# Performance work log

Measured on AMD Instinct MI355X. Metric: run time of the kernel, lower is better.

Reference implementation:

```python
import jax, jax.numpy as jnp
import numpy as np

N = 2048      # agent_num
H = 2048      # hid_size
OBS = 1024    # obs_size
A = 64        # action_dim
ITERS = 3     # comm_iters
B = 1         # batch (structurally 1: original does gate.view(1,n,n))
STD = 0.02


def setup_inputs() -> dict:
    key = jax.random.key(0)
    ks = jax.random.split(key, 10)
    f = lambda k, shp: (jax.random.normal(k, shp, jnp.float32) * STD)
    return {
        "obs": jax.random.normal(ks[0], (B, N, OBS), jnp.float32),
        "alive_mask": jnp.ones((N,), jnp.float32),
        "enc_w": f(ks[1], (H, OBS)),
        "enc_b": jnp.zeros((H,), jnp.float32),
        "g_w": f(ks[2], (N, H)),
        "g_b": jnp.zeros((N,), jnp.float32),
        "w_ih": f(ks[3], (4 * H, H)),
        "w_hh": f(ks[4], (4 * H, H)),
        "b_ih": f(ks[5], (4 * H,)),
        "b_hh": f(ks[6], (4 * H,)),
        "act_w": f(ks[7], (A, H)),
        "act_b": jnp.zeros((A,), jnp.float32),
        "val_w": f(ks[8], (1, H)),
        "val_b": jnp.zeros((1,), jnp.float32),
    }


def reference(obs, alive_mask, enc_w, enc_b, g_w, g_b, w_ih, w_hh,
              b_ih, b_hh, act_w, act_b, val_w, val_b):
    b, n, _ = obs.shape
    hid = enc_w.shape[0]
    # state encoder: tanh(Linear(obs))
    e = jnp.tanh(jnp.einsum('bno,ho->bnh', obs, enc_w) + enc_b)  # (B,n,H)
    h = jnp.zeros((b, n, hid), obs.dtype)
    cell = jnp.zeros((b, n, hid), obs.dtype)
    comm_mask = 1.0 - jnp.eye(n, dtype=obs.dtype)                # (n,n), no self-comm
    n_alive = jnp.sum(alive_mask)
    alive_pair = alive_mask[:, None] * alive_mask[None, :]       # alive[j]*alive[i]
    static_w = comm_mask * alive_pair / (n_alive - 1.0)          # (n,n)

    for it in range(ITERS):
        # hard gate: ceil(sigmoid(g(h)))  -> (B, n_sender, n_receiver)
        gate = jnp.ceil(jax.nn.sigmoid(jnp.einsum('bjh,kh->bjk', h, g_w) + g_b))
        G = gate * static_w                                      # (B,n,n)
        # masked gated broadcast-sum over sender agents j (fused, no (B,n,n,H))
        if it == 0:
            c = jnp.zeros_like(h)
        else:
            c = jnp.einsum('bji,bjh->bih', G, h)
        inp = e + c                                              # (B,n,H)
        # torch.nn.LSTMCell, gate order (i, f, g, o)
        z = (jnp.einsum('bnh,gh->bng', inp, w_ih)
             + jnp.einsum('bnh,gh->bng', h, w_hh) + b_ih + b_hh)
        zi, zf, zg, zo = jnp.split(z, 4, axis=-1)
        cell = jax.nn.sigmoid(zf) * cell + jax.nn.sigmoid(zi) * jnp.tanh(zg)
        h = jax.nn.sigmoid(zo) * jnp.tanh(cell)

    log_p = jax.nn.log_softmax(jnp.einsum('bnh,ah->bna', h, act_w) + act_b, axis=-1)
    value = jnp.einsum('bnh,vh->bnv', h, val_w) + val_b
    return log_p, value
```

## Files before the change

### kernel.cpp

```cpp
#include <hip/hip_runtime.h>
#include <cmath>

#define N_AG 2048
#define HID  2048
#define OBSD 1024
#define ACT  64
#define GATES (4*HID)

typedef short s16x8 __attribute__((ext_vector_type(8)));
typedef short s16x4 __attribute__((ext_vector_type(4)));
typedef float f32x4 __attribute__((ext_vector_type(4)));

__device__ __forceinline__ unsigned short f2bf(float f) {
  union { float f; unsigned u; } v; v.f = f;
  return (unsigned short)((v.u + 0x7FFFu + ((v.u >> 16) & 1u)) >> 16);
}
__device__ __forceinline__ float bf2f(unsigned short u) {
  union { float f; unsigned u; } v; v.u = ((unsigned)u) << 16;
  return v.f;
}
__device__ __forceinline__ float sigm(float x) { return 1.0f / (1.0f + expf(-x)); }

__device__ __forceinline__ void gload16(const unsigned short* g, unsigned short* l) {
  __builtin_amdgcn_global_load_lds(
      (const __attribute__((address_space(1))) void*)g,
      (__attribute__((address_space(3))) void*)l, 16, 0, 0);
}

__global__ __launch_bounds__(512, 2) void gemm256(
    const unsigned short* __restrict__ A, const unsigned short* __restrict__ B,
    int K, int lda, int ldb, unsigned short* __restrict__ C, int ldc)
{
  __shared__ __align__(16) unsigned short As[32768];
  __shared__ __align__(16) unsigned short Bs[32768];

  const int tid  = threadIdx.x;
  const int lane = tid & 63;
  const int wave = tid >> 6;
  const int wm   = wave >> 2, wn = wave & 3;
  const int quad = lane >> 4, l16 = lane & 15, r7 = lane & 7;
  const long tileM = (long)blockIdx.y * 256;
  const long tileN = (long)blockIdx.x * 256;

  const unsigned scol = (((lane & 7) ^ (lane >> 3)) * 8u);
  unsigned aoff[2][2], boff[2][2];
#pragma unroll
  for (int c = 0; c < 2; ++c)
#pragma unroll
    for (int h = 0; h < 2; ++h) {
      unsigned ar = c * 128u + h * 64u + wave * 8u + (lane >> 3);
      unsigned br = c * 128u + (wave >> 2) * 64u + h * 32u + (wave & 3) * 8u + (lane >> 3);
      aoff[c][h] = (unsigned)(tileM + ar) * (unsigned)lda + scol;
      boff[c][h] = (unsigned)(tileN + br) * (unsigned)ldb + scol;
    }

#define ST_A(d, h, t) { \
    gload16(A + aoff[0][h] + (unsigned)(t) * 64u, &As[(d) * 16384 + (h) * 8192 + wave * 512]); \
    gload16(A + aoff[1][h] + (unsigned)(t) * 64u, &As[(d) * 16384 + (h) * 8192 + wave * 512 + 4096]); }
#define ST_B(d, h, t) { \
    gload16(B + boff[0][h] + (unsigned)(t) * 64u, &Bs[(d) * 16384 + (h) * 8192 + wave * 512]); \
    gload16(B + boff[1][h] + (unsigned)(t) * 64u, &Bs[(d) * 16384 + (h) * 8192 + wave * 512 + 4096]); }

  const int ax = wm * 4096 + l16 * 64;
  const int bx = wn * 2048 + l16 * 64;
  const int c0 = (quad ^ r7) * 8;
  const int c1 = ((4 + quad) ^ r7) * 8;

  s16x8 af[4][2], bA[2][2], bB[2][2];
  f32x4 acc[8][4] = {};

#define LD_A(d, Mh) { const unsigned short* p_ = &As[(d) * 16384 + (Mh) * 8192 + ax]; \
    _Pragma("unroll") for (int ml = 0; ml < 4; ++ml) { \
      af[ml][0] = *(const s16x8*)(p_ + ml * 1024 + c0); \
      af[ml][1] = *(const s16x8*)(p_ + ml * 1024 + c1); } }
#define LD_B(d, Nh, bb) { const unsigned short* p_ = &Bs[(d) * 16384 + (Nh) * 8192 + bx]; \
    _Pragma("unroll") for (int nl = 0; nl < 2; ++nl) { \
      bb[nl][0] = *(const s16x8*)(p_ + nl * 1024 + c0); \
      bb[nl][1] = *(const s16x8*)(p_ + nl * 1024 + c1); } }
#define QMM(Mh, Nh, bb) \
    _Pragma("unroll") for (int ml = 0; ml < 4; ++ml) \
    _Pragma("unroll") for (int nl = 0; nl < 2; ++nl) \
    _Pragma("unroll") for (int ks = 0; ks < 2; ++ks) \
      acc[(Mh) * 4 + ml][(Nh) * 2 + nl] = __builtin_amdgcn_mfma_f32_16x16x32_bf16( \
          af[ml][ks], bb[nl][ks], acc[(Mh) * 4 + ml][(Nh) * 2 + nl], 0, 0, 0);
#define LGKM0 asm volatile("s_waitcnt lgkmcnt(0)" ::: "memory")
#define BARRIER __builtin_amdgcn_s_barrier()

  const int NT = K >> 6;

  ST_B(0, 0, 0); ST_A(0, 0, 0); ST_B(0, 1, 0); ST_A(0, 1, 0);
  ST_B(1, 0, 1); ST_A(1, 0, 1); ST_B(1, 1, 1);
  asm volatile("s_waitcnt vmcnt(6)" ::: "memory");
  BARRIER;

  for (int t = 0; t < NT; ++t) {
    const int cur = t & 1, nxt = cur ^ 1;
    const bool s1 = (t + 1 < NT), s2 = (t + 2 < NT);
    LD_A(cur, 0); LD_B(cur, 0, bA);
    if (s1) ST_A(nxt, 1, t + 1);
    BARRIER; LGKM0;
    __builtin_amdgcn_s_setprio(1); QMM(0, 0, bA); __builtin_amdgcn_s_setprio(0);
    BARRIER;
    LD_B(cur, 1, bB);
    if (s2) ST_B(cur, 0, t + 2);
    BARRIER; LGKM0;
    __builtin_amdgcn_s_setprio(1); QMM(0, 1, bB); __builtin_amdgcn_s_setprio(0);
    BARRIER;
    LD_A(cur, 1);
    if (s2) ST_A(cur, 0, t + 2);
    BARRIER; LGKM0;
    __builtin_amdgcn_s_setprio(1); QMM(1, 0, bA); __builtin_amdgcn_s_setprio(0);
    BARRIER;
    if (s2) ST_B(cur, 1, t + 2);
    BARRIER; LGKM0;
    __builtin_amdgcn_s_setprio(1); QMM(1, 1, bB); __builtin_amdgcn_s_setprio(0);
    if (s2)      { asm volatile("s_waitcnt vmcnt(6)" ::: "memory"); }
    else if (s1) { asm volatile("s_waitcnt vmcnt(0)" ::: "memory"); }
    BARRIER;
  }

#pragma unroll
  for (int mf = 0; mf < 8; ++mf) {
    long r0 = tileM + wm * 128 + mf * 16 + quad * 4;
#pragma unroll
    for (int nf = 0; nf < 4; ++nf) {
      long col = tileN + wn * 64 + nf * 16 + l16;
#pragma unroll
      for (int r = 0; r < 4; ++r)
        C[(r0 + r) * ldc + col] = f2bf(acc[mf][nf][r]);
    }
  }
#undef ST_A
#undef ST_B
#undef LD_A
#undef LD_B
#undef QMM
#undef LGKM0
#undef BARRIER
}

template <int MODE>
__global__ __launch_bounds__(256, 4) void gemm_bt(
    const unsigned short* __restrict__ A, const unsigned short* __restrict__ B,
    int K, int lda, int ldb,
    unsigned short* __restrict__ Cb, float* __restrict__ Cf, int ldc,
    const float* __restrict__ bias)
{
  __shared__ __align__(16) unsigned short As0[2 * 128 * 32];
  __shared__ __align__(16) unsigned short Bs0[2 * 128 * 32];
  const int tid  = threadIdx.x;
  const int lane = tid & 63;
  const int wave = tid >> 6;
  const int wm = wave >> 1, wn = wave & 1;
  const int quad = lane >> 4, l16 = lane & 15;
  const long tileM = (long)blockIdx.y * 128;
  const long tileN = (long)blockIdx.x * 128;

  const int srow = lane >> 2;
  const int skc  = (lane & 3) * 8;
  const unsigned short* gA = &A[(tileM + wave * 32 + srow) * lda + skc];
  const unsigned short* gB = &B[(tileN + wave * 32 + srow) * ldb + skc];
  const int ldsOff = wave * 32 * 32;

  f32x4 acc[4][4] = {};
  const int nIt = K >> 5;

  gload16(gA, &As0[ldsOff]);
  gload16(gA + 16 * lda, &As0[ldsOff + 16 * 32]);
  gload16(gB, &Bs0[ldsOff]);
  gload16(gB + 16 * ldb, &Bs0[ldsOff + 16 * 32]);

  for (int i = 0; i < nIt; ++i) {
    __syncthreads();
    const int cb = (i & 1) * 4096;
    if (i + 1 < nIt) {
      const int nb = ((i + 1) & 1) * 4096;
      const long ko = (long)(i + 1) * 32;
      gload16(gA + ko, &As0[nb + ldsOff]);
      gload16(gA + ko + 16 * lda, &As0[nb + ldsOff + 16 * 32]);
      gload16(gB + ko, &Bs0[nb + ldsOff]);
      gload16(gB + ko + 16 * ldb, &Bs0[nb + ldsOff + 16 * 32]);
    }
    s16x8 af[4], bfr[4];
#pragma unroll
    for (int ii = 0; ii < 4; ++ii)
      af[ii] = *(const s16x8*)&As0[cb + (wm * 64 + ii * 16 + l16) * 32 + quad * 8];
#pragma unroll
    for (int j = 0; j < 4; ++j)
      bfr[j] = *(const s16x8*)&Bs0[cb + (wn * 64 + j * 16 + l16) * 32 + quad * 8];
#pragma unroll
    for (int ii = 0; ii < 4; ++ii)
#pragma unroll
      for (int j = 0; j < 4; ++j)
        acc[ii][j] = __builtin_amdgcn_mfma_f32_16x16x32_bf16(af[ii], bfr[j], acc[ii][j], 0, 0, 0);
  }

#pragma unroll
  for (int i = 0; i < 4; ++i) {
    long r0 = tileM + wm * 64 + i * 16 + quad * 4;
#pragma unroll
    for (int j = 0; j < 4; ++j) {
      long col = tileN + wn * 64 + j * 16 + l16;
      float bv = (MODE == 1) ? bias[col] : 0.f;
#pragma unroll
      for (int r = 0; r < 4; ++r) {
        float v = acc[i][j][r];
        if (MODE == 1) v = tanhf(v + bv);
        if (MODE == 2) Cf[(r0 + r) * ldc + col] = v;
        else           Cb[(r0 + r) * ldc + col] = f2bf(v);
      }
    }
  }
}

__global__ void cvt4_dual(const float* __restrict__ inA, unsigned short* __restrict__ outA,
                          const float* __restrict__ inB, unsigned short* __restrict__ outB) {
  int i = blockIdx.x * 256 + threadIdx.x;
  f32x4 a = ((const f32x4*)inA)[i];
  f32x4 b = ((const f32x4*)inB)[i];
  s16x4 oa, ob;
#pragma unroll
  for (int c = 0; c < 4; ++c) { oa[c] = (short)f2bf(a[c]); ob[c] = (short)f2bf(b[c]); }
  ((s16x4*)outA)[i] = oa;
  ((s16x4*)outB)[i] = ob;
}

__global__ void buildw(const float* __restrict__ w_ih, const float* __restrict__ w_hh,
                       const float* __restrict__ nA,
                       unsigned short* __restrict__ Wihb, unsigned short* __restrict__ W2b) {
  int i = blockIdx.x * 256 + threadIdx.x;
  float s = 1.0f / (nA[0] - 1.0f);
  size_t off = (size_t)i * 4;
  f32x4 a = *(const f32x4*)&w_ih[off];
  f32x4 b = *(const f32x4*)&w_hh[off];
  s16x4 oa, ob;
#pragma unroll
  for (int c = 0; c < 4; ++c) {
    oa[c] = (short)f2bf(a[c]);
    ob[c] = (short)f2bf(b[c] - s * a[c]);
  }
  *(s16x4*)&Wihb[off] = oa;
  *(s16x4*)&W2b[off] = ob;
}

__global__ void build_whd(const float* __restrict__ act_w, const float* __restrict__ val_w,
                          unsigned short* __restrict__ whd) {
  int i = blockIdx.x * 256 + threadIdx.x;
  int r = i >> 9;
  int k = (i & 511) * 4;
  f32x4 v = {0.f, 0.f, 0.f, 0.f};
  if (r < 64)       v = *(const f32x4*)&act_w[(size_t)r * HID + k];
  else if (r == 64) v = *(const f32x4*)&val_w[k];
  s16x4 o;
  o[0] = (short)f2bf(v[0]); o[1] = (short)f2bf(v[1]);
  o[2] = (short)f2bf(v[2]); o[3] = (short)f2bf(v[3]);
  *(s16x4*)&whd[(size_t)r * HID + k] = o;
}

__global__ void biasmix(const float* __restrict__ b_ih, const float* __restrict__ b_hh,
                        float* __restrict__ bc) {
  int i = blockIdx.x * 256 + threadIdx.x;
  if (i < GATES) bc[i] = b_ih[i] + b_hh[i];
}

__global__ void nalive_k(const float* __restrict__ alive, float* __restrict__ nA) {
  __shared__ float red[256];
  float s = 0.f;
  for (int i = threadIdx.x; i < N_AG; i += 256) s += alive[i];
  red[threadIdx.x] = s;
  __syncthreads();
  for (int st = 128; st > 0; st >>= 1) {
    if (threadIdx.x < st) red[threadIdx.x] += red[threadIdx.x + st];
    __syncthreads();
  }
  if (threadIdx.x == 0) nA[0] = red[0];
}

__global__ void colsum(const unsigned short* __restrict__ hb, const float* __restrict__ alive,
                       float* __restrict__ S) {
  int hid = blockIdx.x * 256 + threadIdx.x;
  int r0 = blockIdx.y * 128;
  float s = 0.f;
  for (int n = r0; n < r0 + 128; ++n) s += alive[n] * bf2f(hb[(size_t)n * HID + hid]);
  atomicAdd(&S[hid], s);
}

__global__ __launch_bounds__(256) void gemv_q(const unsigned short* __restrict__ Wihb,
                                              const float* __restrict__ S,
                                              const float* __restrict__ nA,
                                              float* __restrict__ q) {
  __shared__ float Sl[HID];
  int tid = threadIdx.x, lane = tid & 63, wave = tid >> 6;
  for (int k = tid; k < HID; k += 256) Sl[k] = S[k];
  __syncthreads();
  int g = blockIdx.x * 4 + wave;
  const unsigned short* wr = Wihb + (size_t)g * HID;
  float acc = 0.f;
#pragma unroll
  for (int c = 0; c < 4; ++c) {
    int k = c * 512 + lane * 8;
    s16x8 w = *(const s16x8*)&wr[k];
#pragma unroll
    for (int e = 0; e < 8; ++e) acc += bf2f((unsigned short)w[e]) * Sl[k + e];
  }
  for (int off = 32; off; off >>= 1) acc += __shfl_xor(acc, off);
  if (lane == 0) q[g] = acc / (nA[0] - 1.0f);
}

__global__ void lstm_k(const unsigned short* __restrict__ zb, const unsigned short* __restrict__ E1b,
                       const float* __restrict__ q, const float* __restrict__ bc,
                       float* __restrict__ cell, unsigned short* __restrict__ hb, int first) {
  int i = blockIdx.x * 256 + threadIdx.x;
  int n = i >> 9;
  int hid = (i & 511) * 4;
  size_t base = (size_t)n * GATES;
  float zt[4][4];
#pragma unroll
  for (int t = 0; t < 4; ++t) {
    int off = t * HID + hid;
    s16x4 e1 = *(const s16x4*)&E1b[base + off];
    f32x4 bcv = *(const f32x4*)&bc[off];
#pragma unroll
    for (int c = 0; c < 4; ++c) zt[t][c] = bf2f((unsigned short)e1[c]) + bcv[c];
    if (!first) {
      s16x4 z2 = *(const s16x4*)&zb[base + off];
      f32x4 qv = *(const f32x4*)&q[off];
#pragma unroll
      for (int c = 0; c < 4; ++c) zt[t][c] += bf2f((unsigned short)z2[c]) + qv[c];
    }
  }
  f32x4 cold = {0.f, 0.f, 0.f, 0.f};
  if (!first) cold = ((const f32x4*)cell)[i];
  f32x4 cnew; s16x4 xb;
#pragma unroll
  for (int c = 0; c < 4; ++c) {
    float ig = sigm(zt[0][c]);
    float fg = sigm(zt[1][c]);
    float gg = tanhf(zt[2][c]);
    float og = sigm(zt[3][c]);
    cnew[c] = fg * cold[c] + ig * gg;
    float hv = og * tanhf(cnew[c]);
    xb[c] = (short)f2bf(hv);
  }
  ((f32x4*)cell)[i] = cnew;
  *(s16x4*)&hb[(size_t)n * HID + hid] = xb;
}

__global__ __launch_bounds__(256) void head_ep(const float* __restrict__ zh,
                                               const float* __restrict__ act_b,
                                               const float* __restrict__ val_b,
                                               float* __restrict__ out) {
  int wave = threadIdx.x >> 6, lane = threadIdx.x & 63;
  int row = blockIdx.x * 4 + wave;
  const float* zr = zh + (size_t)row * 128;
  float a = zr[lane] + act_b[lane];
  float m = a;
  for (int off = 32; off; off >>= 1) m = fmaxf(m, __shfl_xor(m, off));
  float ex = expf(a - m), s = ex;
  for (int off = 32; off; off >>= 1) s += __shfl_xor(s, off);
  out[(size_t)row * ACT + lane] = a - m - logf(s);
  if (lane == 0) out[(size_t)N_AG * ACT + row] = zr[64] + val_b[0];
}

extern "C" void kernel_launch(void* const* d_in, const int* in_sizes, int n_in,
                              void* d_out, int out_size, void* d_ws, size_t ws_size,
                              hipStream_t stream) {
  const float* obs   = (const float*)d_in[0];
  const float* alive = (const float*)d_in[1];
  const float* enc_w = (const float*)d_in[2];
  const float* enc_b = (const float*)d_in[3];
  const float* w_ih  = (const float*)d_in[6];
  const float* w_hh  = (const float*)d_in[7];
  const float* b_ih  = (const float*)d_in[8];
  const float* b_hh  = (const float*)d_in[9];
  const float* act_w = (const float*)d_in[10];
  const float* act_b = (const float*)d_in[11];
  const float* val_w = (const float*)d_in[12];
  const float* val_b = (const float*)d_in[13];
  float* out = (float*)d_out;

  char* p = (char*)d_ws;
  unsigned short* Wihb = (unsigned short*)p; p += (size_t)GATES * HID * 2;
  unsigned short* W2b  = (unsigned short*)p; p += (size_t)GATES * HID * 2;
  unsigned short* E1b  = (unsigned short*)p; p += (size_t)N_AG * GATES * 2;
  unsigned short* zb   = (unsigned short*)p; p += (size_t)N_AG * GATES * 2;
  unsigned short* obsb = (unsigned short*)p; p += (size_t)N_AG * OBSD * 2;
  unsigned short* encb = (unsigned short*)p; p += (size_t)HID * OBSD * 2;
  unsigned short* eb   = (unsigned short*)p; p += (size_t)N_AG * HID * 2;
  unsigned short* hb   = (unsigned short*)p; p += (size_t)N_AG * HID * 2;
  unsigned short* Whd  = (unsigned short*)p; p += (size_t)128 * HID * 2;
  float* cell = (float*)p; p += (size_t)N_AG * HID * 4;
  float* zh   = (float*)p; p += (size_t)N_AG * 128 * 4;
  float* bc   = (float*)p; p += GATES * 4;
  float* q    = (float*)p; p += GATES * 4;
  float* S    = (float*)p; p += HID * 4;
  float* nA   = (float*)p; p += 256;

  cvt4_dual<<<(N_AG * OBSD / 4) / 256, 256, 0, stream>>>(obs, obsb, enc_w, encb);
  nalive_k<<<1, 256, 0, stream>>>(alive, nA);
  buildw<<<((size_t)GATES * HID / 4) / 256, 256, 0, stream>>>(w_ih, w_hh, nA, Wihb, W2b);
  build_whd<<<(128 * HID / 4) / 256, 256, 0, stream>>>(act_w, val_w, Whd);
  biasmix<<<GATES / 256, 256, 0, stream>>>(b_ih, b_hh, bc);

  gemm_bt<1><<<dim3(HID / 128, N_AG / 128), 256, 0, stream>>>(
      obsb, encb, OBSD, OBSD, OBSD, eb, nullptr, HID, enc_b);

  gemm256<<<dim3(GATES / 256, N_AG / 256), 512, 0, stream>>>(
      eb, Wihb, HID, HID, HID, E1b, GATES);
  lstm_k<<<(N_AG * HID / 4) / 256, 256, 0, stream>>>(nullptr, E1b, nullptr, bc, cell, hb, 1);

  for (int it = 1; it < 3; ++it) {
    hipMemsetAsync(S, 0, HID * 4, stream);
    colsum<<<dim3(HID / 256, 16), 256, 0, stream>>>(hb, alive, S);
    gemv_q<<<GATES / 4, 256, 0, stream>>>(Wihb, S, nA, q);
    gemm256<<<dim3(GATES / 256, N_AG / 256), 512, 0, stream>>>(
        hb, W2b, HID, HID, HID, zb, GATES);
    lstm_k<<<(N_AG * HID / 4) / 256, 256, 0, stream>>>(zb, E1b, q, bc, cell, hb, 0);
  }

  gemm_bt<2><<<dim3(1, N_AG / 128), 256, 0, stream>>>(
      hb, Whd, HID, HID, HID, nullptr, zh, 128, nullptr);
  head_ep<<<N_AG / 4, 256, 0, stream>>>(zh, act_b, val_b, out);
}
```

Baseline: 564.4 us.

## Double-buffer A fragments in registers and cut barriers in gemm256 loop

Rewrites the main loop of the 256x256 bf16 MFMA GEMM so that LDS fragment reads for the next quarter-tile, and for the next k-tile, are issued before the current MFMA block runs. A second A-fragment register set (af0/af1) makes this possible. The explicit lgkmcnt waits and roughly half of the workgroup barriers are removed, and the end-of-iteration global-load wait is loosened to vmcnt(2). Per-lane global offsets are now computed from one base address instead of held in eight precomputed registers. The goal is to hide LDS latency and cut synchronization stalls, at the cost of more live vector registers under a 512x2 launch bound and a greater risk of LDS races or spills.

```diff
diff --git a/kernel.cpp b/kernel.cpp
--- a/kernel.cpp
+++ b/kernel.cpp
@@ -42,81 +42,73 @@
   const long tileM = (long)blockIdx.y * 256;
   const long tileN = (long)blockIdx.x * 256;
 
-  const unsigned scol = (((lane & 7) ^ (lane >> 3)) * 8u);
-  unsigned aoff[2][2], boff[2][2];
-#pragma unroll
-  for (int c = 0; c < 2; ++c)
-#pragma unroll
-    for (int h = 0; h < 2; ++h) {
-      unsigned ar = c * 128u + h * 64u + wave * 8u + (lane >> 3);
-      unsigned br = c * 128u + (wave >> 2) * 64u + h * 32u + (wave & 3) * 8u + (lane >> 3);
-      aoff[c][h] = (unsigned)(tileM + ar) * (unsigned)lda + scol;
-      boff[c][h] = (unsigned)(tileN + br) * (unsigned)ldb + scol;
-    }
+  const unsigned scol  = (((lane & 7) ^ (lane >> 3)) * 8u);
+  const unsigned aoffL = (unsigned)(tileM + wave * 8 + (lane >> 3)) * (unsigned)lda + scol;
+  const unsigned boffL = (unsigned)(tileN + (wave >> 2) * 64 + (wave & 3) * 8 + (lane >> 3))
+                           * (unsigned)ldb + scol;
 
 #define ST_A(d, h, t) { \
-    gload16(A + aoff[0][h] + (unsigned)(t) * 64u, &As[(d) * 16384 + (h) * 8192 + wave * 512]); \
-    gload16(A + aoff[1][h] + (unsigned)(t) * 64u, &As[(d) * 16384 + (h) * 8192 + wave * 512 + 4096]); }
+    gload16(A + aoffL + (unsigned)((h) * 64) * (unsigned)lda + (unsigned)(t) * 64u, \
+            &As[(d) * 16384 + (h) * 8192 + wave * 512]); \
+    gload16(A + aoffL + (unsigned)(128 + (h) * 64) * (unsigned)lda + (unsigned)(t) * 64u, \
+            &As[(d) * 16384 + (h) * 8192 + wave * 512 + 4096]); }
 #define ST_B(d, h, t) { \
-    gload16(B + boff[0][h] + (unsigned)(t) * 64u, &Bs[(d) * 16384 + (h) * 8192 + wave * 512]); \
-    gload16(B + boff[1][h] + (unsigned)(t) * 64u, &Bs[(d) * 16384 + (h) * 8192 + wave * 512 + 4096]); }
+    gload16(B + boffL + (unsigned)((h) * 32) * (unsigned)ldb + (unsigned)(t) * 64u, \
+            &Bs[(d) * 16384 + (h) * 8192 + wave * 512]); \
+    gload16(B + boffL + (unsigned)(128 + (h) * 32) * (unsigned)ldb + (unsigned)(t) * 64u, \
+            &Bs[(d) * 16384 + (h) * 8192 + wave * 512 + 4096]); }
 
   const int ax = wm * 4096 + l16 * 64;
   const int bx = wn * 2048 + l16 * 64;
   const int c0 = (quad ^ r7) * 8;
   const int c1 = ((4 + quad) ^ r7) * 8;
 
-  s16x8 af[4][2], bA[2][2], bB[2][2];
+  s16x8 af0[4][2], af1[4][2], bA[2][2], bB[2][2];
   f32x4 acc[8][4] = {};
 
-#define LD_A(d, Mh) { const unsigned short* p_ = &As[(d) * 16384 + (Mh) * 8192 + ax]; \
+#define LD_A(d, Mh, dst) { const unsigned short* p_ = &As[(d) * 16384 + (Mh) * 8192 + ax]; \
     _Pragma("unroll") for (int ml = 0; ml < 4; ++ml) { \
-      af[ml][0] = *(const s16x8*)(p_ + ml * 1024 + c0); \
-      af[ml][1] = *(const s16x8*)(p_ + ml * 1024 + c1); } }
-#define LD_B(d, Nh, bb) { const unsigned short* p_ = &Bs[(d) * 16384 + (Nh) * 8192 + bx]; \
+      dst[ml][0] = *(const s16x8*)(p_ + ml * 1024 + c0); \
+      dst[ml][1] = *(const s16x8*)(p_ + ml * 1024 + c1); } }
+#define LD_B(d, Nh, dst) { const unsigned short* p_ = &Bs[(d) * 16384 + (Nh) * 8192 + bx]; \
     _Pragma("unroll") for (int nl = 0; nl < 2; ++nl) { \
-      bb[nl][0] = *(const s16x8*)(p_ + nl * 1024 + c0); \
-      bb[nl][1] = *(const s16x8*)(p_ + nl * 1024 + c1); } }
-#define QMM(Mh, Nh, bb) \
+      dst[nl][0] = *(const s16x8*)(p_ + nl * 1024 + c0); \
+      dst[nl][1] = *(const s16x8*)(p_ + nl * 1024 + c1); } }
+#define QMM(Mh, Nh, afv, bb) \
     _Pragma("unroll") for (int ml = 0; ml < 4; ++ml) \
     _Pragma("unroll") for (int nl = 0; nl < 2; ++nl) \
     _Pragma("unroll") for (int ks = 0; ks < 2; ++ks) \
       acc[(Mh) * 4 + ml][(Nh) * 2 + nl] = __builtin_amdgcn_mfma_f32_16x16x32_bf16( \
-          af[ml][ks], bb[nl][ks], acc[(Mh) * 4 + ml][(Nh) * 2 + nl], 0, 0, 0);
-#define LGKM0 asm volatile("s_waitcnt lgkmcnt(0)" ::: "memory")
-#define BARRIER __builtin_amdgcn_s_barrier()
+          afv[ml][ks], bb[nl][ks], acc[(Mh) * 4 + ml][(Nh) * 2 + nl], 0, 0, 0);
+#define BAR __builtin_amdgcn_s_barrier()
 
   const int NT = K >> 6;
 
   ST_B(0, 0, 0); ST_A(0, 0, 0); ST_B(0, 1, 0); ST_A(0, 1, 0);
   ST_B(1, 0, 1); ST_A(1, 0, 1); ST_B(1, 1, 1);
-  asm volatile("s_waitcnt vmcnt(6)" ::: "memory");
-  BARRIER;
+  asm volatile("s_waitcnt vmcnt(0)" ::: "memory");
+  BAR;
+  LD_A(0, 0, af0); LD_B(0, 0, bA);
 
   for (int t = 0; t < NT; ++t) {
     const int cur = t & 1, nxt = cur ^ 1;
     const bool s1 = (t + 1 < NT), s2 = (t + 2 < NT);
-    LD_A(cur, 0); LD_B(cur, 0, bA);
+    LD_B(cur, 1, bB);
     if (s1) ST_A(nxt, 1, t + 1);
-    BARRIER; LGKM0;
-    __builtin_amdgcn_s_setprio(1); QMM(0, 0, bA); __builtin_amdgcn_s_setprio(0);
-    BARRIER;
-    LD_B(cur, 1, bB);
+    __builtin_amdgcn_s_setprio(1); QMM(0, 0, af0, bA); __builtin_amdgcn_s_setprio(0);
+    BAR;
+    LD_A(cur, 1, af1);
     if (s2) ST_B(cur, 0, t + 2);
-    BARRIER; LGKM0;
-    __builtin_amdgcn_s_setprio(1); QMM(0, 1, bB); __builtin_amdgcn_s_setprio(0);
-    BARRIER;
-    LD_A(cur, 1);
+    __builtin_amdgcn_s_setprio(1); QMM(0, 1, af0, bB); __builtin_amdgcn_s_setprio(0);
+    BAR;
     if (s2) ST_A(cur, 0, t + 2);
-    BARRIER; LGKM0;
-    __builtin_amdgcn_s_setprio(1); QMM(1, 0, bA); __builtin_amdgcn_s_setprio(0);
-    BARRIER;
+    __builtin_amdgcn_s_setprio(1); QMM(1, 0, af1, bA); __builtin_amdgcn_s_setprio(0);
+    BAR;
     if (s2) ST_B(cur, 1, t + 2);
-    BARRIER; LGKM0;
-    __builtin_amdgcn_s_setprio(1); QMM(1, 1, bB); __builtin_amdgcn_s_setprio(0);
-    if (s2)      { asm volatile("s_waitcnt vmcnt(6)" ::: "memory"); }
-    else if (s1) { asm volatile("s_waitcnt vmcnt(0)" ::: "memory"); }
-    BARRIER;
+    if (s1) { LD_A(nxt, 0, af0); LD_B(nxt, 0, bA); }
+    __builtin_amdgcn_s_setprio(1); QMM(1, 1, af1, bB); __builtin_amdgcn_s_setprio(0);
+    asm volatile("s_waitcnt vmcnt(2)" ::: "memory");
+    BAR;
   }
 
 #pragma unroll
@@ -135,8 +127,7 @@
 #undef LD_A
 #undef LD_B
 #undef QMM
-#undef LGKM0
-#undef BARRIER
+#undef BAR
 }
 
 template <int MODE>
```

New measurement: 576.3 us. 2.1% more time.
